# Kernel optimization log

Measured on AMD Instinct MI355X. Metric: run time of the kernel, lower is better.

Reference implementation:

```python
import jax, jax.numpy as jnp
import numpy as np

N = 4096          # num_nodes
E = 65536         # num edges (avg degree 16)
WALK_LENGTH = 16
OUT_DIM = 8


def setup_inputs() -> dict:
    key = jax.random.key(0)
    k1, k2 = jax.random.split(key, 2)
    edge_index = jax.random.randint(k1, (2, E), 0, N, dtype=jnp.int64)
    # nn.Linear(walk_length, out_dim): weight [out_dim, walk_length], bias [out_dim]
    linear_w = (jax.random.normal(k2, (OUT_DIM, WALK_LENGTH), jnp.float32)
                / np.float32(np.sqrt(WALK_LENGTH)))
    linear_b = jnp.zeros((OUT_DIM,), jnp.float32)
    return {"edge_index": edge_index, "num_nodes": N,
            "linear_w": linear_w, "linear_b": linear_b}


def reference(edge_index, num_nodes, linear_w, linear_b):
    row, col = edge_index[0], edge_index[1]
    # out-degree via scatter_add, clamped to >= 1
    deg = jnp.zeros((num_nodes,), jnp.float32).at[row].add(1.0)
    deg = jnp.maximum(deg, 1.0)
    rw_values = 1.0 / deg[row]                              # [E]
    # random-walk transition matrix P[row, col] = 1/deg[row]
    # (.at[].add sums duplicate edges, matching coalesce())
    P = jnp.zeros((num_nodes, num_nodes), jnp.float32).at[row, col].add(rw_values)
    Pt = P.T

    def step(cur, _):
        cur = Pt @ cur                                      # [N, N]
        return cur, jnp.diagonal(cur)                       # k-step return probs

    cur0 = jnp.eye(num_nodes, dtype=jnp.float32)
    _, diags = jax.lax.scan(step, cur0, None, length=WALK_LENGTH)
    rw_diag = diags.T                                       # [N, walk_length]
    return rw_diag @ linear_w.T + linear_b                  # [N, out_dim]
```

## Files before the change

### kernel.cpp

```cpp
#include <hip/hip_runtime.h>
#include <hip/hip_fp16.h>
#include <hip/hip_fp8.h>

#define NNODES 4096
#define LWALK 16
#define ODIM 8

#define FP8_SCALE 256.0f
#define FP8_INV   0.00390625f
#define FP8_INV2  1.52587890625e-05f

typedef unsigned int uint4n __attribute__((ext_vector_type(4)));
typedef unsigned int uint2n __attribute__((ext_vector_type(2)));
typedef float float2n __attribute__((ext_vector_type(2)));

__device__ __forceinline__ void dec8f(unsigned int lo, unsigned int hi, float* f) {
#if __has_builtin(__builtin_amdgcn_cvt_pk_f32_fp8)
    float2n p;
    p = __builtin_amdgcn_cvt_pk_f32_fp8((int)lo, false); f[0] = p.x; f[1] = p.y;
    p = __builtin_amdgcn_cvt_pk_f32_fp8((int)lo, true);  f[2] = p.x; f[3] = p.y;
    p = __builtin_amdgcn_cvt_pk_f32_fp8((int)hi, false); f[4] = p.x; f[5] = p.y;
    p = __builtin_amdgcn_cvt_pk_f32_fp8((int)hi, true);  f[6] = p.x; f[7] = p.y;
#else
    unsigned int w[2] = {lo, hi};
    const unsigned char* b = (const unsigned char*)w;
#pragma unroll
    for (int i = 0; i < 8; ++i) {
        __hip_fp8_e4m3 t; t.__x = b[i]; f[i] = (float)t;
    }
#endif
}

__device__ __forceinline__ void enc8f(const float* a, unsigned int* lo,
                                      unsigned int* hi) {
#if __has_builtin(__builtin_amdgcn_cvt_pk_fp8_f32)
    int l = 0, h = 0;
    l = __builtin_amdgcn_cvt_pk_fp8_f32(a[0], a[1], l, false);
    l = __builtin_amdgcn_cvt_pk_fp8_f32(a[2], a[3], l, true);
    h = __builtin_amdgcn_cvt_pk_fp8_f32(a[4], a[5], h, false);
    h = __builtin_amdgcn_cvt_pk_fp8_f32(a[6], a[7], h, true);
    *lo = (unsigned int)l; *hi = (unsigned int)h;
#else
    unsigned char b[8];
#pragma unroll
    for (int i = 0; i < 8; ++i)
        b[i] = __hip_cvt_float_to_fp8(a[i], __HIP_SATFINITE, __HIP_E4M3);
    unsigned int w[2];
    __builtin_memcpy(w, b, 8);
    *lo = w[0]; *hi = w[1];
#endif
}

__device__ __forceinline__ void dec16f(uint4n w, float* f) {
    dec8f(w.x, w.y, f);
    dec8f(w.z, w.w, f + 8);
}

__device__ __forceinline__ uint4n enc16f(const float* a) {
    uint4n o;
    unsigned int lo, hi;
    enc8f(a, &lo, &hi);     o.x = lo; o.y = hi;
    enc8f(a + 8, &lo, &hi); o.z = lo; o.w = hi;
    return o;
}

__global__ void detect_fmt_k(const void* ei, int E, int* flag) {
    if (blockIdx.x == 0 && threadIdx.x == 0) {
        const long long* p = (const long long*)ei;
        int ok = 1;
        for (int i = 0; i < 64; ++i) {
            long long v = p[i];
            if (v < 0 || v >= NNODES) { ok = 0; break; }
        }
        *flag = ok;
    }
}

__device__ __forceinline__ int load_idx(const void* p, int i, int fmt) {
    if (fmt) return (int)((const long long*)p)[i];
    return ((const int*)p)[i];
}

__global__ void build_deg_cnt_k(const void* ei, int E, int* deg, int* cnt,
                                const int* fmt) {
    int e = blockIdx.x * blockDim.x + threadIdx.x;
    if (e >= E) return;
    int f = *fmt;
    int r = load_idx(ei, e, f);
    int c = load_idx(ei, E + e, f);
    atomicAdd(&deg[r], 1);
    atomicAdd(&cnt[c], 1);
}

__global__ void scan_k(const int* __restrict__ cnt, int* __restrict__ rowptr,
                       int* __restrict__ cursor) {
    __shared__ int sm[1024];
    int tid = threadIdx.x;
    int v0 = (cnt[4 * tid + 0] + 7) & ~7;
    int v1 = (cnt[4 * tid + 1] + 7) & ~7;
    int v2 = (cnt[4 * tid + 2] + 7) & ~7;
    int v3 = (cnt[4 * tid + 3] + 7) & ~7;
    int tsum = v0 + v1 + v2 + v3;
    sm[tid] = tsum;
    __syncthreads();
    int val = tsum;
    for (int off = 1; off < 1024; off <<= 1) {
        int t = (tid >= off) ? sm[tid - off] : 0;
        __syncthreads();
        val += t;
        sm[tid] = val;
        __syncthreads();
    }
    int excl = val - tsum;
    int p0 = excl, p1 = excl + v0, p2 = p1 + v1, p3 = p2 + v2;
    rowptr[4 * tid + 0] = p0; rowptr[4 * tid + 1] = p1;
    rowptr[4 * tid + 2] = p2; rowptr[4 * tid + 3] = p3;
    cursor[4 * tid + 0] = p0; cursor[4 * tid + 1] = p1;
    cursor[4 * tid + 2] = p2; cursor[4 * tid + 3] = p3;
    if (tid == 1023) rowptr[4096] = val;
}

__global__ void fill_csr_k(const void* ei, int E, const int* __restrict__ deg,
                           int* cursor, uint2* __restrict__ epad, const int* fmt) {
    int e = blockIdx.x * blockDim.x + threadIdx.x;
    if (e >= E) return;
    int f = *fmt;
    int r = load_idx(ei, e, f);
    int c = load_idx(ei, E + e, f);
    int pos = atomicAdd(&cursor[c], 1);
    int d = deg[r];
    float v = 1.0f / (float)(d < 1 ? 1 : d);
    epad[pos] = make_uint2((unsigned)r, __float_as_uint(v));
}

__global__ void pad_fill_k(const int* __restrict__ rowptr,
                           const int* __restrict__ cursor,
                           uint2* __restrict__ epad) {
    int c = blockIdx.x * blockDim.x + threadIdx.x;
    if (c >= NNODES) return;
    for (int p = cursor[c]; p < rowptr[c + 1]; ++p)
        epad[p] = make_uint2(0u, 0u);
}

__global__ void zero_k(uint4n* p) {
    int i = blockIdx.x * blockDim.x + threadIdx.x;
    uint4n z = {0u, 0u, 0u, 0u};
    p[i] = z;
}

__global__ void x1scatter_k(const void* ei, int E, const int* __restrict__ deg,
                            __half* __restrict__ X1, const int* fmt) {
    int e = blockIdx.x * blockDim.x + threadIdx.x;
    if (e >= E) return;
    int f = *fmt;
    int r = load_idx(ei, e, f);
    int c = load_idx(ei, E + e, f);
    int d = deg[r];
    float v = 1.0f / (float)(d < 1 ? 1 : d);
    size_t idx = (size_t)c * NNODES + r;
    unsigned int* base = (unsigned int*)(X1 + (idx & ~(size_t)1));
    bool hi = (idx & 1) != 0;
    unsigned int old = *base, assumed;
    do {
        assumed = old;
        unsigned short cur = hi ? (unsigned short)(assumed >> 16)
                                : (unsigned short)(assumed & 0xFFFFu);
        float nf = __half2float(__ushort_as_half(cur)) + v;
        unsigned short ns = __half_as_ushort(__float2half(nf));
        unsigned int nv = hi ? ((assumed & 0x0000FFFFu) | ((unsigned int)ns << 16))
                             : ((assumed & 0xFFFF0000u) | ns);
        old = atomicCAS(base, assumed, nv);
    } while (old != assumed);
}

__global__ __launch_bounds__(256) void spmm_h8_k(
    const __half* __restrict__ X, unsigned char* __restrict__ Y8,
    const int* __restrict__ rowptr, const uint2* __restrict__ epad,
    float* __restrict__ rw) {
    const int bid = blockIdx.x;
    const int slab = bid & 7;
    const int lane = threadIdx.x & 63;
    const int c =
        __builtin_amdgcn_readfirstlane((bid >> 3) * 4 + (threadIdx.x >> 6));
    const int colo = slab * 512 + lane * 8;
    const __half* Xs = X + colo;
    const int beg = rowptr[c], end = rowptr[c + 1];
    float a[8];
#pragma unroll
    for (int u = 0; u < 8; ++u) a[u] = 0.f;
    for (int e = beg; e < end; e += 8) {
        uint2 ed[8];
#pragma unroll
        for (int j = 0; j < 8; ++j) ed[j] = epad[e + j];
        uint4n x[8];
#pragma unroll
        for (int j = 0; j < 8; ++j)
            x[j] = *(const uint4n*)(Xs + (size_t)ed[j].x * NNODES);
#pragma unroll
        for (int j = 0; j < 8; ++j) {
            float v = __uint_as_float(ed[j].y);
            const __half* h = (const __half*)&x[j];
#pragma unroll
            for (int u = 0; u < 8; ++u)
                a[u] = fmaf(__half2float(h[u]), v, a[u]);
        }
    }
    if ((c >> 9) == slab && lane == ((c & 511) >> 3)) {
        rw[c * LWALK + 0] = __half2float(X[(size_t)c * NNODES + c]);
        float d = 0.f;
#pragma unroll
        for (int u = 0; u < 8; ++u)
            if ((c & 7) == u) d = a[u];
        rw[c * LWALK + 1] = d;
    }
    float s[8];
#pragma unroll
    for (int u = 0; u < 8; ++u) s[u] = a[u] * FP8_SCALE;
    unsigned int lo, hi;
    enc8f(s, &lo, &hi);
    uint2n o;
    o.x = lo; o.y = hi;
    __builtin_nontemporal_store(o, (uint2n*)(Y8 + (size_t)c * NNODES + colo));
}

__global__ __launch_bounds__(256) void fused8_k(
    const unsigned char* __restrict__ X8, unsigned char* __restrict__ Y8,
    const int* __restrict__ rowptr, const uint2* __restrict__ epad,
    float* __restrict__ rw, int kcol,
    const unsigned char* __restrict__ PA, const unsigned char* __restrict__ PB,
    int colO, int colE, int nspmm) {
    __shared__ __half bt[64][66];
    __shared__ __half ct[64][66];
    const int bid = blockIdx.x;
    if (bid < nspmm) {
        const int slab = bid & 3;
        const int lane = threadIdx.x & 63;
        const int c =
            __builtin_amdgcn_readfirstlane((bid >> 2) * 4 + (threadIdx.x >> 6));
        const int colo = slab * 1024 + lane * 16;
        const unsigned char* Xs = X8 + colo;
        const int beg = rowptr[c], end = rowptr[c + 1];
        float a[16];
#pragma unroll
        for (int u = 0; u < 16; ++u) a[u] = 0.f;
        for (int e = beg; e < end; e += 8) {
            uint2 ed[8];
#pragma unroll
            for (int j = 0; j < 8; ++j) ed[j] = epad[e + j];
            uint4n x[8];
#pragma unroll
            for (int j = 0; j < 8; ++j)
                x[j] = *(const uint4n*)(Xs + (size_t)ed[j].x * NNODES);
#pragma unroll
            for (int j = 0; j < 8; ++j) {
                float v = __uint_as_float(ed[j].y);
                float f[16];
                dec16f(x[j], f);
#pragma unroll
                for (int u = 0; u < 16; ++u) a[u] = fmaf(f[u], v, a[u]);
            }
        }
        if ((c >> 10) == slab && lane == ((c & 1023) >> 4)) {
            float d = 0.f;
#pragma unroll
            for (int u = 0; u < 16; ++u)
                if ((c & 15) == u) d = a[u];
            rw[c * LWALK + kcol] = d * FP8_INV;
        }
        uint4n o = enc16f(a);
        __builtin_nontemporal_store(o, (uint4n*)(Y8 + (size_t)c * NNODES + colo));
    } else {
        const int pb = bid - nspmm;
        const int i0 = (pb & 63) * 64;
        const int Jbeg = (pb >> 6) * (NNODES / 16);
        const int Jend = Jbeg + (NNODES / 16);
        const int t = threadIdx.x;
        const int li = t >> 2;
        const int q = t & 3;
        const int c0 = q * 16;
        float accO = 0.f, accE = 0.f;
        for (int J = Jbeg; J < Jend; J += 64) {
            uint4n b16 = __builtin_nontemporal_load(
                (const uint4n*)(PB + (size_t)(J + li) * NNODES + i0 + c0));
            uint4n g16 = __builtin_nontemporal_load(
                (const uint4n*)(PA + (size_t)(J + li) * NNODES + i0 + c0));
            __syncthreads();
            float bf[16], gf[16];
            dec16f(b16, bf);
            dec16f(g16, gf);
#pragma unroll
            for (int s = 0; s < 16; ++s) {
                bt[c0 + s][li] = __float2half(bf[s]);
                ct[c0 + s][li] = __float2half(gf[s]);
            }
            __syncthreads();
            uint4n a16 = __builtin_nontemporal_load(
                (const uint4n*)(PA + (size_t)(i0 + li) * NNODES + J + c0));
            float af[16];
            dec16f(a16, af);
#pragma unroll
            for (int s = 0; s < 16; ++s) {
                accO = fmaf(af[s], __half2float(bt[li][c0 + s]), accO);
                accE = fmaf(af[s], __half2float(ct[li][c0 + s]), accE);
            }
        }
        accO += __shfl_xor(accO, 1);
        accO += __shfl_xor(accO, 2);
        accE += __shfl_xor(accE, 1);
        accE += __shfl_xor(accE, 2);
        if (q == 0) {
            atomicAdd(&rw[(i0 + li) * LWALK + colO], accO * FP8_INV2);
            atomicAdd(&rw[(i0 + li) * LWALK + colE], accE * FP8_INV2);
        }
    }
}

__global__ void linear_k(const float* __restrict__ rw, const float* __restrict__ W,
                         const float* __restrict__ b, float* __restrict__ out) {
    int i = blockIdx.x * blockDim.x + threadIdx.x;
    if (i >= NNODES * ODIM) return;
    int s = i >> 3, d = i & 7;
    float acc = b[d];
#pragma unroll
    for (int k = 0; k < LWALK; ++k)
        acc = fmaf(rw[s * LWALK + k], W[d * LWALK + k], acc);
    out[i] = acc;
}

extern "C" void kernel_launch(void* const* d_in, const int* in_sizes, int n_in,
                              void* d_out, int out_size, void* d_ws, size_t ws_size,
                              hipStream_t stream) {
    const void* ei = d_in[0];
    int E = in_sizes[0] / 2;
    const float* W = (const float*)d_in[2];
    const float* bias = (const float*)d_in[3];
    float* out = (float*)d_out;

    char* ws = (char*)d_ws;
    size_t off = 0;
    auto alloc = [&](size_t bytes) -> char* {
        char* p = ws + off;
        off = (off + bytes + 255) & ~(size_t)255;
        return p;
    };
    int* flag = (int*)alloc(4);
    int* deg = (int*)alloc(NNODES * 4);
    int* cnt = (int*)alloc(NNODES * 4);
    int* rowptr = (int*)alloc((NNODES + 1) * 4);
    int* cursor = (int*)alloc(NNODES * 4);
    uint2* epad = (uint2*)alloc(((size_t)E + 8 * NNODES) * 8);
    float* rw = (float*)alloc(NNODES * LWALK * 4);
    __half* Xh = (__half*)alloc((size_t)NNODES * NNODES * 2);
    unsigned char* A = (unsigned char*)alloc((size_t)NNODES * NNODES);
    unsigned char* B = (unsigned char*)alloc((size_t)NNODES * NNODES);
    unsigned char* C = (unsigned char*)alloc((size_t)NNODES * NNODES);

    (void)hipMemsetAsync(deg, 0, NNODES * 4, stream);
    (void)hipMemsetAsync(cnt, 0, NNODES * 4, stream);
    (void)hipMemsetAsync(rw, 0, NNODES * LWALK * 4, stream);
    detect_fmt_k<<<1, 64, 0, stream>>>(ei, E, flag);
    build_deg_cnt_k<<<(E + 255) / 256, 256, 0, stream>>>(ei, E, deg, cnt, flag);
    scan_k<<<1, 1024, 0, stream>>>(cnt, rowptr, cursor);
    fill_csr_k<<<(E + 255) / 256, 256, 0, stream>>>(ei, E, deg, cursor, epad, flag);
    pad_fill_k<<<(NNODES + 255) / 256, 256, 0, stream>>>(rowptr, cursor, epad);

    zero_k<<<NNODES * (NNODES / 8) / 256, 256, 0, stream>>>((uint4n*)Xh);
    x1scatter_k<<<(E + 255) / 256, 256, 0, stream>>>(ei, E, deg, Xh, flag);

    spmm_h8_k<<<NNODES * 8 / 4, 256, 0, stream>>>(Xh, A, rowptr, epad, rw);

    const int SG = 4096;
    fused8_k<<<SG, 256, 0, stream>>>(A, B, rowptr, epad, rw, 2, nullptr, nullptr, 0, 0, SG);
    fused8_k<<<SG, 256, 0, stream>>>(B, C, rowptr, epad, rw, 3, nullptr, nullptr, 0, 0, SG);
    fused8_k<<<SG, 256, 0, stream>>>(C, A, rowptr, epad, rw, 4, nullptr, nullptr, 0, 0, SG);
    fused8_k<<<SG + 1024, 256, 0, stream>>>(A, B, rowptr, epad, rw, 5, A, C, 8, 9, SG);
    fused8_k<<<SG + 1024, 256, 0, stream>>>(B, C, rowptr, epad, rw, 6, B, A, 10, 11, SG);
    fused8_k<<<SG + 1024, 256, 0, stream>>>(C, A, rowptr, epad, rw, 7, C, B, 12, 13, SG);
    fused8_k<<<1024, 256, 0, stream>>>(nullptr, nullptr, rowptr, epad, rw, 0, A, C, 14, 15, 0);

    linear_k<<<(NNODES * ODIM + 255) / 256, 256, 0, stream>>>(rw, W, bias, out);
}
```

Measured before the change: 322.7 us.

## Build two-step walk matrix directly from CSR via shared-memory row accumulation

Drops the dense fp16 P^T materialisation (a 32 MB zero fill, an atomic-CAS scatter, and a dense-input SpMM). Each block instead computes one row of P^T·P^T by walking two levels of the CSR adjacency and accumulating into a shared-memory float row. It also records diagonal entries for steps 1 and 2, then writes the row out as fp8. This removes a large amount of memory traffic in exchange for shared-memory atomics and load imbalance that grows with degree squared.

```diff
diff --git a/kernel.cpp b/kernel.cpp
--- a/kernel.cpp
+++ b/kernel.cpp
@@ -142,85 +142,42 @@
         epad[p] = make_uint2(0u, 0u);
 }
 
-__global__ void zero_k(uint4n* p) {
-    int i = blockIdx.x * blockDim.x + threadIdx.x;
-    uint4n z = {0u, 0u, 0u, 0u};
-    p[i] = z;
-}
-
-__global__ void x1scatter_k(const void* ei, int E, const int* __restrict__ deg,
-                            __half* __restrict__ X1, const int* fmt) {
-    int e = blockIdx.x * blockDim.x + threadIdx.x;
-    if (e >= E) return;
-    int f = *fmt;
-    int r = load_idx(ei, e, f);
-    int c = load_idx(ei, E + e, f);
-    int d = deg[r];
-    float v = 1.0f / (float)(d < 1 ? 1 : d);
-    size_t idx = (size_t)c * NNODES + r;
-    unsigned int* base = (unsigned int*)(X1 + (idx & ~(size_t)1));
-    bool hi = (idx & 1) != 0;
-    unsigned int old = *base, assumed;
-    do {
-        assumed = old;
-        unsigned short cur = hi ? (unsigned short)(assumed >> 16)
-                                : (unsigned short)(assumed & 0xFFFFu);
-        float nf = __half2float(__ushort_as_half(cur)) + v;
-        unsigned short ns = __half_as_ushort(__float2half(nf));
-        unsigned int nv = hi ? ((assumed & 0x0000FFFFu) | ((unsigned int)ns << 16))
-                             : ((assumed & 0xFFFF0000u) | ns);
-        old = atomicCAS(base, assumed, nv);
-    } while (old != assumed);
-}
-
-__global__ __launch_bounds__(256) void spmm_h8_k(
-    const __half* __restrict__ X, unsigned char* __restrict__ Y8,
+__global__ __launch_bounds__(256) void x2build_k(
     const int* __restrict__ rowptr, const uint2* __restrict__ epad,
-    float* __restrict__ rw) {
-    const int bid = blockIdx.x;
-    const int slab = bid & 7;
-    const int lane = threadIdx.x & 63;
-    const int c =
-        __builtin_amdgcn_readfirstlane((bid >> 3) * 4 + (threadIdx.x >> 6));
-    const int colo = slab * 512 + lane * 8;
-    const __half* Xs = X + colo;
+    unsigned char* __restrict__ Y8, float* __restrict__ rw) {
+    __shared__ float row[NNODES];
+    __shared__ float dia1;
+    const int c = blockIdx.x;
+    const int t = threadIdx.x;
+    for (int i = t; i < NNODES; i += 256) row[i] = 0.f;
+    if (t == 0) dia1 = 0.f;
+    __syncthreads();
     const int beg = rowptr[c], end = rowptr[c + 1];
-    float a[8];
-#pragma unroll
-    for (int u = 0; u < 8; ++u) a[u] = 0.f;
-    for (int e = beg; e < end; e += 8) {
-        uint2 ed[8];
-#pragma unroll
-        for (int j = 0; j < 8; ++j) ed[j] = epad[e + j];
-        uint4n x[8];
-#pragma unroll
-        for (int j = 0; j < 8; ++j)
-            x[j] = *(const uint4n*)(Xs + (size_t)ed[j].x * NNODES);
-#pragma unroll
-        for (int j = 0; j < 8; ++j) {
-            float v = __uint_as_float(ed[j].y);
-            const __half* h = (const __half*)&x[j];
-#pragma unroll
-            for (int u = 0; u < 8; ++u)
-                a[u] = fmaf(__half2float(h[u]), v, a[u]);
-        }
-    }
-    if ((c >> 9) == slab && lane == ((c & 511) >> 3)) {
-        rw[c * LWALK + 0] = __half2float(X[(size_t)c * NNODES + c]);
-        float d = 0.f;
-#pragma unroll
-        for (int u = 0; u < 8; ++u)
-            if ((c & 7) == u) d = a[u];
-        rw[c * LWALK + 1] = d;
-    }
-    float s[8];
-#pragma unroll
-    for (int u = 0; u < 8; ++u) s[u] = a[u] * FP8_SCALE;
-    unsigned int lo, hi;
-    enc8f(s, &lo, &hi);
-    uint2n o;
-    o.x = lo; o.y = hi;
-    __builtin_nontemporal_store(o, (uint2n*)(Y8 + (size_t)c * NNODES + colo));
+    for (int i1 = beg + t; i1 < end; i1 += 256) {
+        uint2 e1 = epad[i1];
+        float v = __uint_as_float(e1.y);
+        if (v != 0.f) {
+            int r = (int)e1.x;
+            if (r == c) atomicAdd(&dia1, v);
+            int b2 = rowptr[r], n2 = rowptr[r + 1];
+            for (int j = b2; j < n2; ++j) {
+                uint2 e2 = epad[j];
+                float w = __uint_as_float(e2.y);
+                if (w != 0.f) atomicAdd(&row[e2.x], v * w);
+            }
+        }
+    }
+    __syncthreads();
+    if (t == 0) {
+        rw[c * LWALK + 0] = dia1;
+        rw[c * LWALK + 1] = row[c];
+    }
+    float f[16];
+    const int base = t * 16;
+#pragma unroll
+    for (int u = 0; u < 16; ++u) f[u] = row[base + u] * FP8_SCALE;
+    uint4n o = enc16f(f);
+    __builtin_nontemporal_store(o, (uint4n*)(Y8 + (size_t)c * NNODES + base));
 }
 
 __global__ __launch_bounds__(256) void fused8_k(
@@ -350,7 +307,6 @@
     int* cursor = (int*)alloc(NNODES * 4);
     uint2* epad = (uint2*)alloc(((size_t)E + 8 * NNODES) * 8);
     float* rw = (float*)alloc(NNODES * LWALK * 4);
-    __half* Xh = (__half*)alloc((size_t)NNODES * NNODES * 2);
     unsigned char* A = (unsigned char*)alloc((size_t)NNODES * NNODES);
     unsigned char* B = (unsigned char*)alloc((size_t)NNODES * NNODES);
     unsigned char* C = (unsigned char*)alloc((size_t)NNODES * NNODES);
@@ -364,10 +320,7 @@
     fill_csr_k<<<(E + 255) / 256, 256, 0, stream>>>(ei, E, deg, cursor, epad, flag);
     pad_fill_k<<<(NNODES + 255) / 256, 256, 0, stream>>>(rowptr, cursor, epad);
 
-    zero_k<<<NNODES * (NNODES / 8) / 256, 256, 0, stream>>>((uint4n*)Xh);
-    x1scatter_k<<<(E + 255) / 256, 256, 0, stream>>>(ei, E, deg, Xh, flag);
-
-    spmm_h8_k<<<NNODES * 8 / 4, 256, 0, stream>>>(Xh, A, rowptr, epad, rw);
+    x2build_k<<<NNODES, 256, 0, stream>>>(rowptr, epad, A, rw);
 
     const int SG = 4096;
     fused8_k<<<SG, 256, 0, stream>>>(A, B, rowptr, epad, rw, 2, nullptr, nullptr, 0, 0, SG);
```

Measured after the change: 304.8 us. 1.06x faster.
